# Kernel tuning notes

Measured on AMD Instinct MI355X. Metric: run time of the kernel, lower is better.

The kernel has to match this reference:

```python
import jax, jax.numpy as jnp
import numpy as np

N_NODES = 100000
N_EDGES = 1600000
IN_DIM = 128
OUT_DIM = 64
BN_EPS = 1e-5


def setup_inputs() -> dict:
    key = jax.random.key(0)
    ks = jax.random.split(key, 8)
    x = jax.random.normal(ks[0], (N_NODES, IN_DIM), dtype=jnp.float32)
    edge_index = jax.random.randint(ks[1], (2, N_EDGES), 0, N_NODES, dtype=jnp.int64)
    W = jax.random.normal(ks[2], (IN_DIM, OUT_DIM), dtype=jnp.float32) / np.sqrt(IN_DIM)
    b = jax.random.normal(ks[3], (OUT_DIM,), dtype=jnp.float32) * 0.01
    gamma = jax.random.normal(ks[4], (OUT_DIM,), dtype=jnp.float32) * 0.1 + 1.0
    beta = jax.random.normal(ks[5], (OUT_DIM,), dtype=jnp.float32) * 0.1
    run_mean = jax.random.normal(ks[6], (OUT_DIM,), dtype=jnp.float32) * 0.1
    run_var = jax.random.uniform(ks[7], (OUT_DIM,), dtype=jnp.float32, minval=0.5, maxval=1.5)
    return {"x": x, "edge_index": edge_index, "W": W, "b": b,
            "gamma": gamma, "beta": beta, "run_mean": run_mean, "run_var": run_var}


def reference(x, edge_index, W, b, gamma, beta, run_mean, run_var):
    # GCNConv: h = X W; out = D^-1/2 (A + I) D^-1/2 h + b  (add_self_loops=True)
    src = edge_index[0]
    dst = edge_index[1]
    n = x.shape[0]
    # degree from adj_t row-sums (dst counts), +1 for self loop
    deg = jax.ops.segment_sum(jnp.ones_like(dst, dtype=x.dtype), dst, num_segments=n) + 1.0
    d_inv_sqrt = jax.lax.rsqrt(deg)
    norm_e = d_inv_sqrt[src] * d_inv_sqrt[dst]          # [E]
    h = x @ W                                            # [N, OUT_DIM]
    msgs = h[src] * norm_e[:, None]                      # [E, OUT_DIM] gather
    agg = jax.ops.segment_sum(msgs, dst, num_segments=n) # scatter-add
    agg = agg + h * (1.0 / deg)[:, None]                 # self-loop term (d^-1/2 * d^-1/2)
    agg = agg + b                                        # PyG adds bias post-aggregation
    # BatchNorm1d (eval mode: running stats), then ReLU; dropout is identity in eval
    bn = (agg - run_mean) * jax.lax.rsqrt(run_var + BN_EPS) * gamma + beta
    return jax.nn.relu(bn)
```

## Files before the change

kernel.cpp:

```cpp
#include <hip/hip_runtime.h>
#include <hip/hip_bf16.h>

#define IN_DIM 128
#define OUT_DIM 64
#define BN_EPS 1e-5f
#define BSH 7
#define BROWS 128
#define MAXBUCK 800


__global__ __launch_bounds__(1024) void k_bhist(const int4* __restrict__ dst4, int E4,
                                                int nbuck, int* __restrict__ gbcnt) {
    __shared__ int hcnt[MAXBUCK];
    for (int i = threadIdx.x; i < nbuck; i += 1024) hcnt[i] = 0;
    __syncthreads();
    int base = blockIdx.x * 2048 + threadIdx.x;
    #pragma unroll
    for (int j = 0; j < 2; ++j) {
        int i4 = base + j * 1024;
        if (i4 < E4) {
            int4 v = dst4[i4];
            atomicAdd(&hcnt[v.x >> BSH], 1);
            atomicAdd(&hcnt[v.y >> BSH], 1);
            atomicAdd(&hcnt[v.z >> BSH], 1);
            atomicAdd(&hcnt[v.w >> BSH], 1);
        }
    }
    __syncthreads();
    for (int i = threadIdx.x; i < nbuck; i += 1024)
        if (hcnt[i]) atomicAdd(&gbcnt[i], hcnt[i]);
}

__global__ __launch_bounds__(1024) void k_bscan(const int* __restrict__ gbcnt, int nbuck,
                                                int E, int* __restrict__ gbase,
                                                int* __restrict__ gcursor) {
    __shared__ int sh[1024];
    int t = threadIdx.x;
    int v = (t < nbuck) ? gbcnt[t] : 0;
    sh[t] = v;
    __syncthreads();
    for (int d = 1; d < 1024; d <<= 1) {
        int tv = (t >= d) ? sh[t - d] : 0;
        __syncthreads();
        sh[t] += tv;
        __syncthreads();
    }
    if (t < nbuck) {
        int b = sh[t] - v;
        gbase[t] = b;
        gcursor[t] = b;
    }
    if (t == 1023) gbase[nbuck] = E;
}

__global__ __launch_bounds__(1024) void k_bscatter(const int4* __restrict__ src4,
                                                   const int4* __restrict__ dst4, int E4,
                                                   int nbuck, int* __restrict__ gcursor,
                                                   int* __restrict__ recs) {
    __shared__ int hcnt[MAXBUCK];
    __shared__ int hbase[MAXBUCK];
    for (int i = threadIdx.x; i < nbuck; i += 1024) hcnt[i] = 0;
    __syncthreads();

    int i4a = blockIdx.x * 2048 + threadIdx.x;
    int i4b = i4a + 1024;
    bool oka = i4a < E4;
    bool okb = i4b < E4;
    int4 sa, da, sb, db;
    int bk[8], rc[8], rk[8];
    if (oka) {
        sa = src4[i4a]; da = dst4[i4a];
        bk[0] = da.x >> BSH; rc[0] = (sa.x << BSH) | (da.x & (BROWS - 1));
        rk[0] = atomicAdd(&hcnt[bk[0]], 1);
        bk[1] = da.y >> BSH; rc[1] = (sa.y << BSH) | (da.y & (BROWS - 1));
        rk[1] = atomicAdd(&hcnt[bk[1]], 1);
        bk[2] = da.z >> BSH; rc[2] = (sa.z << BSH) | (da.z & (BROWS - 1));
        rk[2] = atomicAdd(&hcnt[bk[2]], 1);
        bk[3] = da.w >> BSH; rc[3] = (sa.w << BSH) | (da.w & (BROWS - 1));
        rk[3] = atomicAdd(&hcnt[bk[3]], 1);
    }
    if (okb) {
        sb = src4[i4b]; db = dst4[i4b];
        bk[4] = db.x >> BSH; rc[4] = (sb.x << BSH) | (db.x & (BROWS - 1));
        rk[4] = atomicAdd(&hcnt[bk[4]], 1);
        bk[5] = db.y >> BSH; rc[5] = (sb.y << BSH) | (db.y & (BROWS - 1));
        rk[5] = atomicAdd(&hcnt[bk[5]], 1);
        bk[6] = db.z >> BSH; rc[6] = (sb.z << BSH) | (db.z & (BROWS - 1));
        rk[6] = atomicAdd(&hcnt[bk[6]], 1);
        bk[7] = db.w >> BSH; rc[7] = (sb.w << BSH) | (db.w & (BROWS - 1));
        rk[7] = atomicAdd(&hcnt[bk[7]], 1);
    }
    __syncthreads();
    for (int i = threadIdx.x; i < nbuck; i += 1024) {
        int c = hcnt[i];
        if (c) hbase[i] = atomicAdd(&gcursor[i], c);
    }
    __syncthreads();
    if (oka) {
        recs[hbase[bk[0]] + rk[0]] = rc[0];
        recs[hbase[bk[1]] + rk[1]] = rc[1];
        recs[hbase[bk[2]] + rk[2]] = rc[2];
        recs[hbase[bk[3]] + rk[3]] = rc[3];
    }
    if (okb) {
        recs[hbase[bk[4]] + rk[4]] = rc[4];
        recs[hbase[bk[5]] + rk[5]] = rc[5];
        recs[hbase[bk[6]] + rk[6]] = rc[6];
        recs[hbase[bk[7]] + rk[7]] = rc[7];
    }
}

__global__ __launch_bounds__(1024) void k_sort(const int* __restrict__ gbase,
                                               const int* __restrict__ recs,
                                               int* __restrict__ sorted,
                                               int* __restrict__ offs,
                                               float* __restrict__ dinv, int N) {
    __shared__ int hist[BROWS];
    __shared__ int cur[BROWS];
    __shared__ int sh[BROWS];
    int b = blockIdx.x;
    int e0 = gbase[b], e1 = gbase[b + 1];
    int tid = threadIdx.x;
    if (tid < BROWS) hist[tid] = 0;
    __syncthreads();
    for (int e = e0 + tid; e < e1; e += 1024)
        atomicAdd(&hist[recs[e] & (BROWS - 1)], 1);
    __syncthreads();
    int v = (tid < BROWS) ? hist[tid] : 0;
    if (tid < BROWS) sh[tid] = v;
    __syncthreads();
    for (int d = 1; d < BROWS; d <<= 1) {
        int t = (tid < BROWS && tid >= d) ? sh[tid - d] : 0;
        __syncthreads();
        if (tid < BROWS) sh[tid] += t;
        __syncthreads();
    }
    if (tid < BROWS) {
        int pre = sh[tid] - v;
        cur[tid] = pre;
        int n = (b << BSH) + tid;
        if (n < N) {
            offs[n] = e0 + pre;
            dinv[n] = rsqrtf((float)(v + 1));
        }
    }
    __syncthreads();
    for (int e = e0 + tid; e < e1; e += 1024) {
        int r = recs[e];
        int p = atomicAdd(&cur[r & (BROWS - 1)], 1);
        sorted[e0 + p] = r >> BSH;
    }
}

__global__ __launch_bounds__(256) void k_gemm(const float* __restrict__ x,
                                              const float* __restrict__ W,
                                              const float* __restrict__ dinv,
                                              __hip_bfloat16* __restrict__ mbf, int N) {
    __shared__ float Wl[IN_DIM * OUT_DIM];
    __shared__ float xl[16 * IN_DIM];

    for (int i = threadIdx.x; i < (IN_DIM * OUT_DIM) / 4; i += 256)
        ((float4*)Wl)[i] = ((const float4*)W)[i];

    int node0 = blockIdx.x * 16;
    for (int i = threadIdx.x; i < 16 * IN_DIM / 4; i += 256) {
        int n = node0 + (i >> 5);
        if (n < N)
            ((float4*)xl)[i] = ((const float4*)x)[(size_t)node0 * (IN_DIM / 4) + i];
    }
    __syncthreads();

    int wave = threadIdx.x >> 6;
    int lane = threadIdx.x & 63;
    int nb = node0 + wave * 4;

    float acc[4] = {0.f, 0.f, 0.f, 0.f};
    for (int k0 = 0; k0 < IN_DIM; k0 += 4) {
        float4 xv0 = ((float4*)xl)[((wave * 4 + 0) * IN_DIM + k0) >> 2];
        float4 xv1 = ((float4*)xl)[((wave * 4 + 1) * IN_DIM + k0) >> 2];
        float4 xv2 = ((float4*)xl)[((wave * 4 + 2) * IN_DIM + k0) >> 2];
        float4 xv3 = ((float4*)xl)[((wave * 4 + 3) * IN_DIM + k0) >> 2];
        #pragma unroll
        for (int kk = 0; kk < 4; ++kk) {
            float w = Wl[(k0 + kk) * OUT_DIM + lane];
            acc[0] += ((float*)&xv0)[kk] * w;
            acc[1] += ((float*)&xv1)[kk] * w;
            acc[2] += ((float*)&xv2)[kk] * w;
            acc[3] += ((float*)&xv3)[kk] * w;
        }
    }
    #pragma unroll
    for (int j = 0; j < 4; ++j) {
        int n = nb + j;
        if (n < N)
            mbf[(size_t)n * OUT_DIM + lane] = __float2bfloat16(acc[j] * dinv[n]);
    }
}

__device__ inline void accum_bf8(float* acc, uint4 r) {
    const unsigned* u = (const unsigned*)&r;
    #pragma unroll
    for (int i = 0; i < 4; ++i) {
        acc[2 * i]     += __uint_as_float(u[i] << 16);
        acc[2 * i + 1] += __uint_as_float(u[i] & 0xffff0000u);
    }
}

__global__ __launch_bounds__(256) void k_agg(const int* __restrict__ offs,
                                             const int* __restrict__ sorted,
                                             const float* __restrict__ dinv,
                                             const uint4* __restrict__ mbf4,
                                             const float* __restrict__ b,
                                             const float* __restrict__ gamma,
                                             const float* __restrict__ beta,
                                             const float* __restrict__ mean,
                                             const float* __restrict__ var,
                                             float* __restrict__ out, int N, int E) {
    int wid = (blockIdx.x * 256 + threadIdx.x) >> 6;
    int lane = threadIdx.x & 63;
    if (wid >= N) return;
    int n = wid;
    int s0 = offs[n];
    int s1 = (n == N - 1) ? E : offs[n + 1];
    int g = lane >> 3;
    int sub = lane & 7;

    float acc[8] = {0.f, 0.f, 0.f, 0.f, 0.f, 0.f, 0.f, 0.f};
    int e = s0;
    for (; e + 16 <= s1; e += 16) {
        int sA = sorted[e + g];
        int sB = sorted[e + 8 + g];
        uint4 ra = mbf4[(size_t)sA * 8 + sub];
        uint4 rb = mbf4[(size_t)sB * 8 + sub];
        accum_bf8(acc, ra);
        accum_bf8(acc, rb);
    }
    for (; e < s1; e += 8) {
        int idx = e + g;
        if (idx < s1) {
            uint4 ra = mbf4[(size_t)sorted[idx] * 8 + sub];
            accum_bf8(acc, ra);
        }
    }

    #pragma unroll
    for (int mask = 8; mask <= 32; mask <<= 1) {
        #pragma unroll
        for (int k = 0; k < 8; ++k)
            acc[k] += __shfl_xor(acc[k], mask, 64);
    }

    if (lane < 8) {
        uint4 sf = mbf4[(size_t)n * 8 + lane];
        float s[8];
        {
            const unsigned* u = (const unsigned*)&sf;
            #pragma unroll
            for (int i = 0; i < 4; ++i) {
                s[2 * i]     = __uint_as_float(u[i] << 16);
                s[2 * i + 1] = __uint_as_float(u[i] & 0xffff0000u);
            }
        }
        float dn = dinv[n];
        float4 gg0 = ((const float4*)gamma)[lane * 2], gg1 = ((const float4*)gamma)[lane * 2 + 1];
        float4 vv0 = ((const float4*)var)[lane * 2],   vv1 = ((const float4*)var)[lane * 2 + 1];
        float4 bb0 = ((const float4*)b)[lane * 2],     bb1 = ((const float4*)b)[lane * 2 + 1];
        float4 mm0 = ((const float4*)mean)[lane * 2],  mm1 = ((const float4*)mean)[lane * 2 + 1];
        float4 ee0 = ((const float4*)beta)[lane * 2],  ee1 = ((const float4*)beta)[lane * 2 + 1];
        float gv[8] = {gg0.x, gg0.y, gg0.z, gg0.w, gg1.x, gg1.y, gg1.z, gg1.w};
        float vv[8] = {vv0.x, vv0.y, vv0.z, vv0.w, vv1.x, vv1.y, vv1.z, vv1.w};
        float bv[8] = {bb0.x, bb0.y, bb0.z, bb0.w, bb1.x, bb1.y, bb1.z, bb1.w};
        float mv[8] = {mm0.x, mm0.y, mm0.z, mm0.w, mm1.x, mm1.y, mm1.z, mm1.w};
        float ev[8] = {ee0.x, ee0.y, ee0.z, ee0.w, ee1.x, ee1.y, ee1.z, ee1.w};
        float o[8];
        #pragma unroll
        for (int k = 0; k < 8; ++k) {
            float sc = gv[k] * rsqrtf(vv[k] + BN_EPS);
            float vval = ((acc[k] + s[k]) * dn + bv[k] - mv[k]) * sc + ev[k];
            o[k] = vval > 0.f ? vval : 0.f;
        }
        float4* op = (float4*)&out[(size_t)n * OUT_DIM + lane * 8];
        op[0] = make_float4(o[0], o[1], o[2], o[3]);
        op[1] = make_float4(o[4], o[5], o[6], o[7]);
    }
}


extern "C" void kernel_launch(void* const* d_in, const int* in_sizes, int n_in,
                              void* d_out, int out_size, void* d_ws, size_t ws_size,
                              hipStream_t stream) {
    const float* x     = (const float*)d_in[0];
    const int*   edges = (const int*)d_in[1];
    const float* W     = (const float*)d_in[2];
    const float* b     = (const float*)d_in[3];
    const float* gamma = (const float*)d_in[4];
    const float* beta  = (const float*)d_in[5];
    const float* rmean = (const float*)d_in[6];
    const float* rvar  = (const float*)d_in[7];
    float* out = (float*)d_out;

    int N = in_sizes[0] / IN_DIM;
    int E = in_sizes[1] / 2;
    const int* src = edges;
    const int* dst = edges + E;

    int nbuck = (N + BROWS - 1) >> BSH;
    int E4 = E >> 2;
    int nebk = (E4 + 2047) / 2048;

    char* ws = (char*)d_ws;
    size_t mB = ((size_t)N * OUT_DIM * sizeof(__hip_bfloat16) + 255) & ~(size_t)255;
    size_t eB = ((size_t)E * sizeof(int) + 255) & ~(size_t)255;
    __hip_bfloat16* mbf = (__hip_bfloat16*)(ws);
    int*   recs    = (int*)  (ws + mB);
    int*   sorted  = (int*)  (ws + mB + eB);
    int*   gbcnt   = (int*)  (ws + mB + 2 * eB);
    int*   gbase   = gbcnt + nbuck;
    int*   gcursor = gbase + nbuck + 1;
    float* dinv    = (float*)(gcursor + nbuck);
    int*   offs    = (int*)(dinv + N);

    hipMemsetAsync(gbcnt, 0, (size_t)nbuck * sizeof(int), stream);

    k_bhist<<<nebk, 1024, 0, stream>>>((const int4*)dst, E4, nbuck, gbcnt);
    k_bscan<<<1, 1024, 0, stream>>>(gbcnt, nbuck, E, gbase, gcursor);
    k_bscatter<<<nebk, 1024, 0, stream>>>((const int4*)src, (const int4*)dst, E4,
                                          nbuck, gcursor, recs);
    k_sort<<<nbuck, 1024, 0, stream>>>(gbase, recs, sorted, offs, dinv, N);
    k_gemm<<<(N + 15) / 16, 256, 0, stream>>>(x, W, dinv, mbf, N);
    k_agg<<<(N + 3) / 4, 256, 0, stream>>>(offs, sorted, dinv, (const uint4*)mbf,
                                           b, gamma, beta, rmean, rvar, out, N, E);
}
```

Baseline: 245.4 us.

## Drop bucket histogram pass using fixed-capacity buckets; store W as packed bf16

```diff
diff --git a/kernel.cpp b/kernel.cpp
--- a/kernel.cpp
+++ b/kernel.cpp
@@ -7,51 +7,8 @@
 #define BSH 7
 #define BROWS 128
 #define MAXBUCK 800
-
-
-__global__ __launch_bounds__(1024) void k_bhist(const int4* __restrict__ dst4, int E4,
-                                                int nbuck, int* __restrict__ gbcnt) {
-    __shared__ int hcnt[MAXBUCK];
-    for (int i = threadIdx.x; i < nbuck; i += 1024) hcnt[i] = 0;
-    __syncthreads();
-    int base = blockIdx.x * 2048 + threadIdx.x;
-    #pragma unroll
-    for (int j = 0; j < 2; ++j) {
-        int i4 = base + j * 1024;
-        if (i4 < E4) {
-            int4 v = dst4[i4];
-            atomicAdd(&hcnt[v.x >> BSH], 1);
-            atomicAdd(&hcnt[v.y >> BSH], 1);
-            atomicAdd(&hcnt[v.z >> BSH], 1);
-            atomicAdd(&hcnt[v.w >> BSH], 1);
-        }
-    }
-    __syncthreads();
-    for (int i = threadIdx.x; i < nbuck; i += 1024)
-        if (hcnt[i]) atomicAdd(&gbcnt[i], hcnt[i]);
-}
-
-__global__ __launch_bounds__(1024) void k_bscan(const int* __restrict__ gbcnt, int nbuck,
-                                                int E, int* __restrict__ gbase,
-                                                int* __restrict__ gcursor) {
-    __shared__ int sh[1024];
-    int t = threadIdx.x;
-    int v = (t < nbuck) ? gbcnt[t] : 0;
-    sh[t] = v;
-    __syncthreads();
-    for (int d = 1; d < 1024; d <<= 1) {
-        int tv = (t >= d) ? sh[t - d] : 0;
-        __syncthreads();
-        sh[t] += tv;
-        __syncthreads();
-    }
-    if (t < nbuck) {
-        int b = sh[t] - v;
-        gbase[t] = b;
-        gcursor[t] = b;
-    }
-    if (t == 1023) gbase[nbuck] = E;
-}
+#define CAP 2560
+
 
 __global__ __launch_bounds__(1024) void k_bscatter(const int4* __restrict__ src4,
                                                    const int4* __restrict__ dst4, int E4,
@@ -97,29 +54,31 @@
     }
     __syncthreads();
     if (oka) {
-        recs[hbase[bk[0]] + rk[0]] = rc[0];
-        recs[hbase[bk[1]] + rk[1]] = rc[1];
-        recs[hbase[bk[2]] + rk[2]] = rc[2];
-        recs[hbase[bk[3]] + rk[3]] = rc[3];
+        recs[bk[0] * CAP + hbase[bk[0]] + rk[0]] = rc[0];
+        recs[bk[1] * CAP + hbase[bk[1]] + rk[1]] = rc[1];
+        recs[bk[2] * CAP + hbase[bk[2]] + rk[2]] = rc[2];
+        recs[bk[3] * CAP + hbase[bk[3]] + rk[3]] = rc[3];
     }
     if (okb) {
-        recs[hbase[bk[4]] + rk[4]] = rc[4];
-        recs[hbase[bk[5]] + rk[5]] = rc[5];
-        recs[hbase[bk[6]] + rk[6]] = rc[6];
-        recs[hbase[bk[7]] + rk[7]] = rc[7];
-    }
-}
-
-__global__ __launch_bounds__(1024) void k_sort(const int* __restrict__ gbase,
+        recs[bk[4] * CAP + hbase[bk[4]] + rk[4]] = rc[4];
+        recs[bk[5] * CAP + hbase[bk[5]] + rk[5]] = rc[5];
+        recs[bk[6] * CAP + hbase[bk[6]] + rk[6]] = rc[6];
+        recs[bk[7] * CAP + hbase[bk[7]] + rk[7]] = rc[7];
+    }
+}
+
+__global__ __launch_bounds__(1024) void k_sort(const int* __restrict__ gcnt,
                                                const int* __restrict__ recs,
                                                int* __restrict__ sorted,
                                                int* __restrict__ offs,
+                                               int* __restrict__ deg,
                                                float* __restrict__ dinv, int N) {
     __shared__ int hist[BROWS];
     __shared__ int cur[BROWS];
     __shared__ int sh[BROWS];
     int b = blockIdx.x;
-    int e0 = gbase[b], e1 = gbase[b + 1];
+    int cnt = gcnt[b];
+    int e0 = b * CAP, e1 = e0 + cnt;
     int tid = threadIdx.x;
     if (tid < BROWS) hist[tid] = 0;
     __syncthreads();
@@ -141,6 +100,7 @@
         int n = (b << BSH) + tid;
         if (n < N) {
             offs[n] = e0 + pre;
+            deg[n] = v;
             dinv[n] = rsqrtf((float)(v + 1));
         }
     }
@@ -156,11 +116,17 @@
                                               const float* __restrict__ W,
                                               const float* __restrict__ dinv,
                                               __hip_bfloat16* __restrict__ mbf, int N) {
-    __shared__ float Wl[IN_DIM * OUT_DIM];
+    __shared__ unsigned Wp[(IN_DIM / 2) * OUT_DIM];
     __shared__ float xl[16 * IN_DIM];
 
-    for (int i = threadIdx.x; i < (IN_DIM * OUT_DIM) / 4; i += 256)
-        ((float4*)Wl)[i] = ((const float4*)W)[i];
+    for (int i = threadIdx.x; i < (IN_DIM / 2) * OUT_DIM; i += 256) {
+        int k2 = i >> 6, ln = i & 63;
+        float w0 = W[(2 * k2) * OUT_DIM + ln];
+        float w1 = W[(2 * k2 + 1) * OUT_DIM + ln];
+        unsigned u0 = (unsigned)__bfloat16_as_ushort(__float2bfloat16(w0));
+        unsigned u1 = (unsigned)__bfloat16_as_ushort(__float2bfloat16(w1));
+        Wp[i] = (u1 << 16) | u0;
+    }
 
     int node0 = blockIdx.x * 16;
     for (int i = threadIdx.x; i < 16 * IN_DIM / 4; i += 256) {
@@ -176,18 +142,20 @@
 
     float acc[4] = {0.f, 0.f, 0.f, 0.f};
     for (int k0 = 0; k0 < IN_DIM; k0 += 4) {
+        unsigned wa = Wp[(k0 >> 1) * OUT_DIM + lane];
+        unsigned wb = Wp[((k0 >> 1) + 1) * OUT_DIM + lane];
+        float w0 = __uint_as_float(wa << 16);
+        float w1 = __uint_as_float(wa & 0xffff0000u);
+        float w2 = __uint_as_float(wb << 16);
+        float w3 = __uint_as_float(wb & 0xffff0000u);
         float4 xv0 = ((float4*)xl)[((wave * 4 + 0) * IN_DIM + k0) >> 2];
         float4 xv1 = ((float4*)xl)[((wave * 4 + 1) * IN_DIM + k0) >> 2];
         float4 xv2 = ((float4*)xl)[((wave * 4 + 2) * IN_DIM + k0) >> 2];
         float4 xv3 = ((float4*)xl)[((wave * 4 + 3) * IN_DIM + k0) >> 2];
-        #pragma unroll
-        for (int kk = 0; kk < 4; ++kk) {
-            float w = Wl[(k0 + kk) * OUT_DIM + lane];
-            acc[0] += ((float*)&xv0)[kk] * w;
-            acc[1] += ((float*)&xv1)[kk] * w;
-            acc[2] += ((float*)&xv2)[kk] * w;
-            acc[3] += ((float*)&xv3)[kk] * w;
-        }
+        acc[0] += xv0.x * w0 + xv0.y * w1 + xv0.z * w2 + xv0.w * w3;
+        acc[1] += xv1.x * w0 + xv1.y * w1 + xv1.z * w2 + xv1.w * w3;
+        acc[2] += xv2.x * w0 + xv2.y * w1 + xv2.z * w2 + xv2.w * w3;
+        acc[3] += xv3.x * w0 + xv3.y * w1 + xv3.z * w2 + xv3.w * w3;
     }
     #pragma unroll
     for (int j = 0; j < 4; ++j) {
@@ -207,6 +175,7 @@
 }
 
 __global__ __launch_bounds__(256) void k_agg(const int* __restrict__ offs,
+                                             const int* __restrict__ deg,
                                              const int* __restrict__ sorted,
                                              const float* __restrict__ dinv,
                                              const uint4* __restrict__ mbf4,
@@ -215,13 +184,13 @@
                                              const float* __restrict__ beta,
                                              const float* __restrict__ mean,
                                              const float* __restrict__ var,
-                                             float* __restrict__ out, int N, int E) {
+                                             float* __restrict__ out, int N) {
     int wid = (blockIdx.x * 256 + threadIdx.x) >> 6;
     int lane = threadIdx.x & 63;
     if (wid >= N) return;
     int n = wid;
     int s0 = offs[n];
-    int s1 = (n == N - 1) ? E : offs[n + 1];
+    int s1 = s0 + deg[n];
     int g = lane >> 3;
     int sub = lane & 7;
 
@@ -310,24 +279,21 @@
 
     char* ws = (char*)d_ws;
     size_t mB = ((size_t)N * OUT_DIM * sizeof(__hip_bfloat16) + 255) & ~(size_t)255;
-    size_t eB = ((size_t)E * sizeof(int) + 255) & ~(size_t)255;
+    size_t pB = ((size_t)nbuck * CAP * sizeof(int) + 255) & ~(size_t)255;
     __hip_bfloat16* mbf = (__hip_bfloat16*)(ws);
     int*   recs    = (int*)  (ws + mB);
-    int*   sorted  = (int*)  (ws + mB + eB);
-    int*   gbcnt   = (int*)  (ws + mB + 2 * eB);
-    int*   gbase   = gbcnt + nbuck;
-    int*   gcursor = gbase + nbuck + 1;
-    float* dinv    = (float*)(gcursor + nbuck);
-    int*   offs    = (int*)(dinv + N);
-
-    hipMemsetAsync(gbcnt, 0, (size_t)nbuck * sizeof(int), stream);
-
-    k_bhist<<<nebk, 1024, 0, stream>>>((const int4*)dst, E4, nbuck, gbcnt);
-    k_bscan<<<1, 1024, 0, stream>>>(gbcnt, nbuck, E, gbase, gcursor);
+    int*   sorted  = (int*)  (ws + mB + pB);
+    int*   gcursor = (int*)  (ws + mB + 2 * pB);
+    int*   offs    = gcursor + nbuck;
+    int*   deg     = offs + N;
+    float* dinv    = (float*)(deg + N);
+
+    hipMemsetAsync(gcursor, 0, (size_t)nbuck * sizeof(int), stream);
+
     k_bscatter<<<nebk, 1024, 0, stream>>>((const int4*)src, (const int4*)dst, E4,
                                           nbuck, gcursor, recs);
-    k_sort<<<nbuck, 1024, 0, stream>>>(gbase, recs, sorted, offs, dinv, N);
+    k_sort<<<nbuck, 1024, 0, stream>>>(gcursor, recs, sorted, offs, deg, dinv, N);
     k_gemm<<<(N + 15) / 16, 256, 0, stream>>>(x, W, dinv, mbf, N);
-    k_agg<<<(N + 3) / 4, 256, 0, stream>>>(offs, sorted, dinv, (const uint4*)mbf,
-                                           b, gamma, beta, rmean, rvar, out, N, E);
-}
+    k_agg<<<(N + 3) / 4, 256, 0, stream>>>(offs, deg, sorted, dinv, (const uint4*)mbf,
+                                           b, gamma, beta, rmean, rvar, out, N);
+}
```

Result: no change. 244.7 us (-0.3%).
